# Kernel optimization log

Hardware: AMD Instinct MI355X
Metric: run time of the kernel (lower is better)

The kernel has to match this reference:

```python
import jax, jax.numpy as jnp
import numpy as np

K_HIDDEN = 512
N_POS = 24
N_COLOR = 6
EPS = 1e-5


def setup_inputs() -> dict:
    key = jax.random.key(0)
    k1, k2 = jax.random.split(key)
    B = 1024
    x = jax.random.normal(k1, (B, N_POS, N_COLOR * K_HIDDEN), dtype=jnp.float32)
    # kaiming-uniform-ish scale for the (k_out, k_in, 2) weight
    fan_in = K_HIDDEN * 2
    bound = float(np.sqrt(6.0 / fan_in))
    conv_weight = jax.random.uniform(k2, (K_HIDDEN, K_HIDDEN, 2), dtype=jnp.float32,
                                     minval=-bound, maxval=bound)
    conv_bias = jnp.zeros((K_HIDDEN,), dtype=jnp.float32)
    norm_weight = jnp.ones((K_HIDDEN,), dtype=jnp.float32)
    norm_bias = jnp.zeros((K_HIDDEN,), dtype=jnp.float32)
    return {"x": x, "conv_weight": conv_weight, "conv_bias": conv_bias,
            "norm_weight": norm_weight, "norm_bias": norm_bias}


def _color_layernorm(x, gamma, beta):
    # x: (B, 24, 6*k); normalize over the full channel axis, affine tied per block of 6
    mean = jnp.mean(x, axis=-1, keepdims=True)
    var = jnp.mean(jnp.square(x - mean), axis=-1, keepdims=True)  # unbiased=False
    xn = (x - mean) * jax.lax.rsqrt(var + EPS)
    xn = xn.reshape(*x.shape[:-1], K_HIDDEN, N_COLOR)
    xn = xn * gamma[:, None] + beta[:, None]
    return xn.reshape(x.shape)


def _color_conv(x, weight, bias):
    # x: (B, 24, 6*k) -> (B, 24, k, 6)
    B = x.shape[0]
    xr = x.reshape(B, N_POS, K_HIDDEN, N_COLOR)
    alpha = weight[:, :, 0] - weight[:, :, 1]   # (k_out, k_in)
    beta_w = weight[:, :, 1]                    # (k_out, k_in)
    term1 = jnp.einsum('bikd,ok->biod', xr, alpha)      # per-color linear
    x_sum = xr.sum(axis=3)                               # (B, 24, k_in)
    term2 = jnp.einsum('bik,ok->bio', x_sum, beta_w)     # color-sum linear
    out = term1 + term2[..., None] + bias[None, None, :, None]
    return out.reshape(B, N_POS, K_HIDDEN * N_COLOR)


def reference(x, conv_weight, conv_bias, norm_weight, norm_bias):
    h = _color_layernorm(x, norm_weight, norm_bias)
    h = _color_conv(h, conv_weight, conv_bias)
    return x + jax.nn.relu(h)
```

## Files before the change

### kernel.cpp

```cpp
#include <hip/hip_runtime.h>
#include <stdint.h>
#include <stddef.h>

#define KH   512
#define DF   3072
#define EPSF 1e-5f
#define PPB  8
#define ROWS 48
#define TSS  516

typedef __attribute__((ext_vector_type(4))) float f32x4;
typedef __attribute__((ext_vector_type(2))) float f32x2;
typedef __attribute__((ext_vector_type(8))) short bf16x8;
typedef __attribute__((ext_vector_type(4))) unsigned int u32x4;

__device__ __forceinline__ unsigned short f2bf(float f) {
  union { float f; unsigned u; } c; c.f = f;
  unsigned u = c.u;
  u += 0x7fffu + ((u >> 16) & 1u);
  return (unsigned short)(u >> 16);
}
__device__ __forceinline__ unsigned short f2bf_trunc(float f) {
  union { float f; unsigned u; } c; c.f = f;
  return (unsigned short)(c.u >> 16);
}
__device__ __forceinline__ float bf2f(unsigned short u) {
  union { unsigned u; float f; } c; c.u = ((unsigned)u) << 16;
  return c.f;
}
__device__ __forceinline__ float bfl(unsigned u) {
  union { unsigned u; float f; } c; c.u = u << 16;
  return c.f;
}
__device__ __forceinline__ float bfh(unsigned u) {
  union { unsigned u; float f; } c; c.u = u & 0xffff0000u;
  return c.f;
}

__global__ __launch_bounds__(256) void prep_w(const float* __restrict__ cw,
                                              const float* __restrict__ cb,
                                              const float* __restrict__ nw,
                                              const float* __restrict__ nb,
                                              unsigned char* __restrict__ wbt,
                                              float* __restrict__ c12) {
  const int o = blockIdx.x;
  const int t = threadIdx.x;
  const int wn = o >> 6, nn = (o >> 4) & 3, co = o & 15;
  float c1 = 0.f, c2 = 0.f;
  for (int k = t; k < KH; k += 256) {
    float w0 = cw[o * 1024 + 2 * k];
    float w1 = cw[o * 1024 + 2 * k + 1];
    float a  = w0 - w1;
    float g  = nw[k], b = nb[k];
    int s = k >> 5, kin = k & 31, h = kin >> 3, e = kin & 7;
    size_t base = (size_t)(((wn * 16 + s) * 4 + nn)) * 1024 + (h * 16 + co) * 16 + e * 2;
    *(unsigned short*)(wbt + base)          = f2bf(a * g);
    *(unsigned short*)(wbt + base + 524288) = f2bf(w1 * g);
    float tt = a + 6.f * w1;
    c1 += tt * b;
    c2 += tt * g;
  }
  #pragma unroll
  for (int off = 32; off >= 1; off >>= 1) {
    c1 += __shfl_xor(c1, off);
    c2 += __shfl_xor(c2, off);
  }
  __shared__ float s1[4], s2[4];
  int wid = t >> 6, lane = t & 63;
  if (lane == 0) { s1[wid] = c1; s2[wid] = c2; }
  __syncthreads();
  if (t == 0) {
    c12[o]      = s1[0] + s1[1] + s1[2] + s1[3] + cb[o];
    c12[KH + o] = s2[0] + s2[1] + s2[2] + s2[3];
  }
}

__global__ __launch_bounds__(512, 4) void fused_main(
    const float* __restrict__ x,
    const unsigned char* __restrict__ wbt,
    const float* __restrict__ c12,
    float* __restrict__ out)
{
  __shared__ unsigned char As[ROWS * 1024];
  __shared__ unsigned char Sx[PPB * 1024];
  __shared__ float Ts[PPB * TSS];
  __shared__ float st[PPB * 2];

  const int tid  = threadIdx.x;
  const int lane = tid & 63;
  const int wid  = tid >> 6;
  const int co   = lane & 15;
  const int h    = lane >> 4;
  const int rvb  = h << 2;
  const size_t r0 = (size_t)blockIdx.x * PPB;

  const unsigned char* wA = wbt + (size_t)wid * 65536;
  bf16x8 bvA[4], bvB[4];

  {
    const float* xb = x + r0 * DF;
    f32x4 q[12];
    #pragma unroll
    for (int i = 0; i < 12; i++) q[i] = *(const f32x4*)(xb + i * 2048 + tid * 4);

    #pragma unroll
    for (int n = 0; n < 4; n++)
      bvA[n] = *(const bf16x8*)(wA + n * 1024 + lane * 16);

    #pragma unroll
    for (int i = 0; i < 12; i++) {
      int base = i * 2048 + tid * 4;
      int pl   = base / 3072;
      int rem  = base - pl * 3072;
      int k0   = rem / 6;
      int d0   = rem - k0 * 6;
      #pragma unroll
      for (int e = 0; e < 4; e++) {
        int d = d0 + e, k = k0;
        if (d >= 6) { d -= 6; k += 1; }
        int row  = pl * 6 + d;
        int byte = row * 1024 + ((((k >> 3) ^ (row & 7)) << 4)) + (k & 7) * 2;
        *(unsigned short*)(As + byte) = f2bf_trunc(q[i][e]);
      }
    }
  }
  __syncthreads();

  {
    float vals[48];
    #pragma unroll
    for (int d = 0; d < 6; d++) {
      int row = wid * 6 + d;
      u32x4 v = *(const u32x4*)(As + row * 1024 + ((lane ^ (row & 7)) << 4));
      #pragma unroll
      for (int jj = 0; jj < 4; jj++) {
        vals[d * 8 + 2 * jj]     = bfl(v[jj]);
        vals[d * 8 + 2 * jj + 1] = bfh(v[jj]);
      }
    }
    float s = 0.f, sq = 0.f;
    #pragma unroll
    for (int i = 0; i < 48; i++) { s += vals[i]; sq += vals[i] * vals[i]; }
    #pragma unroll
    for (int off = 32; off >= 1; off >>= 1) {
      s  += __shfl_xor(s,  off);
      sq += __shfl_xor(sq, off);
    }
    float mean = s * (1.f / 3072.f);
    float var  = sq * (1.f / 3072.f) - mean * mean;
    float rstd = rsqrtf(var + EPSF);
    if (lane == 0) { st[2 * wid] = mean; st[2 * wid + 1] = rstd; }
    bf16x8 sv;
    #pragma unroll
    for (int g = 0; g < 8; g++) {
      float ss = vals[g] + vals[8 + g] + vals[16 + g] + vals[24 + g] +
                 vals[32 + g] + vals[40 + g];
      sv[g] = (short)f2bf(ss);
    }
    *(bf16x8*)(Sx + wid * 1024 + ((lane ^ (wid & 7)) << 4)) = sv;
  }
  __syncthreads();

  f32x4 acc1[3][4];
  #pragma unroll
  for (int m = 0; m < 3; m++)
    #pragma unroll
    for (int n = 0; n < 4; n++) acc1[m][n] = (f32x4){0.f, 0.f, 0.f, 0.f};

  int arow[3], ar7[3];
  #pragma unroll
  for (int m = 0; m < 3; m++) {
    int row = m * 16 + co;
    arow[m] = row * 1024;  ar7[m] = row & 7;
  }

  {
    bf16x8 afA[3], afB[3];
    #pragma unroll
    for (int m = 0; m < 3; m++)
      afA[m] = *(const bf16x8*)(As + arow[m] + ((h ^ ar7[m]) << 4));

    #pragma unroll 1
    for (int s = 0; s < 16; s += 2) {
      {
        int g6 = (s + 1) * 4 + h;
        #pragma unroll
        for (int m = 0; m < 3; m++)
          afB[m] = *(const bf16x8*)(As + arow[m] + ((g6 ^ ar7[m]) << 4));
        const unsigned char* pn = wA + (size_t)(s + 1) * 4096;
        #pragma unroll
        for (int n = 0; n < 4; n++)
          bvB[n] = *(const bf16x8*)(pn + n * 1024 + lane * 16);
      }
      #pragma unroll
      for (int m = 0; m < 3; m++)
        #pragma unroll
        for (int n = 0; n < 4; n++)
          acc1[m][n] = __builtin_amdgcn_mfma_f32_16x16x32_bf16(afA[m], bvA[n], acc1[m][n], 0, 0, 0);
      if (s + 2 < 16) {
        int g6 = (s + 2) * 4 + h;
        #pragma unroll
        for (int m = 0; m < 3; m++)
          afA[m] = *(const bf16x8*)(As + arow[m] + ((g6 ^ ar7[m]) << 4));
        const unsigned char* pn2 = wA + (size_t)(s + 2) * 4096;
        #pragma unroll
        for (int n = 0; n < 4; n++)
          bvA[n] = *(const bf16x8*)(pn2 + n * 1024 + lane * 16);
      }
      #pragma unroll
      for (int m = 0; m < 3; m++)
        #pragma unroll
        for (int n = 0; n < 4; n++)
          acc1[m][n] = __builtin_amdgcn_mfma_f32_16x16x32_bf16(afB[m], bvB[n], acc1[m][n], 0, 0, 0);
    }
  }

  {
    f32x4 acc2[4];
    #pragma unroll
    for (int n = 0; n < 4; n++) acc2[n] = (f32x4){0.f, 0.f, 0.f, 0.f};
    const unsigned char* wB2 = wbt + 524288 + (size_t)wid * 65536;
    const int sxr = (co & 7);
    bf16x8 cA[4], cB[4];
    bf16x8 a2A, a2B;
    #pragma unroll
    for (int n = 0; n < 4; n++)
      cA[n] = *(const bf16x8*)(wB2 + n * 1024 + lane * 16);
    a2A = *(const bf16x8*)(Sx + sxr * 1024 + ((h ^ sxr) << 4));

    #pragma unroll 1
    for (int s = 0; s < 16; s += 2) {
      {
        int g6 = (s + 1) * 4 + h;
        a2B = *(const bf16x8*)(Sx + sxr * 1024 + ((g6 ^ sxr) << 4));
        const unsigned char* pn = wB2 + (size_t)(s + 1) * 4096;
        #pragma unroll
        for (int n = 0; n < 4; n++)
          cB[n] = *(const bf16x8*)(pn + n * 1024 + lane * 16);
      }
      #pragma unroll
      for (int n = 0; n < 4; n++)
        acc2[n] = __builtin_amdgcn_mfma_f32_16x16x32_bf16(a2A, cA[n], acc2[n], 0, 0, 0);
      if (s + 2 < 16) {
        int g6 = (s + 2) * 4 + h;
        a2A = *(const bf16x8*)(Sx + sxr * 1024 + ((g6 ^ sxr) << 4));
        const unsigned char* pn2 = wB2 + (size_t)(s + 2) * 4096;
        #pragma unroll
        for (int n = 0; n < 4; n++)
          cA[n] = *(const bf16x8*)(pn2 + n * 1024 + lane * 16);
      }
      #pragma unroll
      for (int n = 0; n < 4; n++)
        acc2[n] = __builtin_amdgcn_mfma_f32_16x16x32_bf16(a2B, cB[n], acc2[n], 0, 0, 0);
    }
    if (h < 2) {
      #pragma unroll
      for (int n = 0; n < 4; n++)
        #pragma unroll
        for (int v = 0; v < 4; v++)
          Ts[(rvb + v) * TSS + wid * 64 + n * 16 + co] = acc2[n][v];
    }
  }

  #pragma unroll
  for (int n = 0; n < 4; n++) {
    const int o = wid * 64 + n * 16 + co;
    const float C1 = c12[o];
    const float C2 = c12[KH + o];
    const int swzo = o >> 3;
    const int ob2 = (o & 7) * 2;
    #pragma unroll
    for (int m = 0; m < 3; m++) {
      int j0  = m * 16 + rvb;
      int pl0 = j0 / 6;
      int d0  = j0 - pl0 * 6;
      float mean0 = st[2 * pl0], rstd0 = st[2 * pl0 + 1];
      float t20   = Ts[pl0 * TSS + o];
      float cc0   = C1 - mean0 * rstd0 * C2;
      if (d0 < 3) {
        f32x4 ov;
        #pragma unroll
        for (int v = 0; v < 4; v++) {
          int j = j0 + v;
          unsigned short rx = *(const unsigned short*)(
              As + j * 1024 + ((swzo ^ (j & 7)) << 4) + ob2);
          ov[v] = bf2f(rx) + fmaxf(rstd0 * (acc1[m][n][v] + t20) + cc0, 0.f);
        }
        *(f32x4*)(out + (r0 + pl0) * DF + o * 6 + d0) = ov;
      } else {
        int pl1 = pl0 + 1;
        float mean1 = st[2 * pl1], rstd1 = st[2 * pl1 + 1];
        float t21   = Ts[pl1 * TSS + o];
        float cc1   = C1 - mean1 * rstd1 * C2;
        f32x2 o0, o1;
        #pragma unroll
        for (int v = 0; v < 2; v++) {
          int j = j0 + v;
          unsigned short rx = *(const unsigned short*)(
              As + j * 1024 + ((swzo ^ (j & 7)) << 4) + ob2);
          o0[v] = bf2f(rx) + fmaxf(rstd0 * (acc1[m][n][v] + t20) + cc0, 0.f);
        }
        #pragma unroll
        for (int v = 2; v < 4; v++) {
          int j = j0 + v;
          unsigned short rx = *(const unsigned short*)(
              As + j * 1024 + ((swzo ^ (j & 7)) << 4) + ob2);
          o1[v - 2] = bf2f(rx) + fmaxf(rstd1 * (acc1[m][n][v] + t21) + cc1, 0.f);
        }
        *(f32x2*)(out + (r0 + pl0) * DF + o * 6 + 4) = o0;
        *(f32x2*)(out + (r0 + pl1) * DF + o * 6)     = o1;
      }
    }
  }
}

extern "C" void kernel_launch(void* const* d_in, const int* in_sizes, int n_in,
                              void* d_out, int out_size, void* d_ws, size_t ws_size,
                              hipStream_t stream) {
  (void)n_in; (void)out_size; (void)ws_size;
  const float* x  = (const float*)d_in[0];
  const float* cw = (const float*)d_in[1];
  const float* cb = (const float*)d_in[2];
  const float* nw = (const float*)d_in[3];
  const float* nb = (const float*)d_in[4];
  float* out = (float*)d_out;

  unsigned char* wbt = (unsigned char*)d_ws;
  float* c12 = (float*)((char*)d_ws + (size_t)1024 * 1024);

  prep_w<<<512, 256, 0, stream>>>(cw, cb, nw, nb, wbt, c12);

  const int R = in_sizes[0] / DF;
  fused_main<<<R / PPB, 512, 0, stream>>>(x, wbt, c12, out);
}
```

Before: 238.4 us.

## Load one row per wave directly and drop scattered LDS staging pass

Each wave now loads its own position row contiguously, 48 floats per lane, and computes LayerNorm statistics and color sums straight from registers. It then writes the bf16 A tile with vectorized 16-byte LDS stores instead of per-element 2-byte scattered stores, and one __syncthreads plus the LDS re-read are removed. It also wraps the MFMA bursts in s_setprio to favour matrix issue over competing waves. The global load pattern per instruction changes from fully coalesced across the block to per-lane 192-byte strided chunks. The color sum now uses truncating rather than rounding bf16 conversion, which slightly changes numerics.

```diff
diff --git a/kernel.cpp b/kernel.cpp
--- a/kernel.cpp
+++ b/kernel.cpp
@@ -12,7 +12,6 @@
 typedef __attribute__((ext_vector_type(4))) float f32x4;
 typedef __attribute__((ext_vector_type(2))) float f32x2;
 typedef __attribute__((ext_vector_type(8))) short bf16x8;
-typedef __attribute__((ext_vector_type(4))) unsigned int u32x4;
 
 __device__ __forceinline__ unsigned short f2bf(float f) {
   union { float f; unsigned u; } c; c.f = f;
@@ -26,14 +25,6 @@
 }
 __device__ __forceinline__ float bf2f(unsigned short u) {
   union { unsigned u; float f; } c; c.u = ((unsigned)u) << 16;
-  return c.f;
-}
-__device__ __forceinline__ float bfl(unsigned u) {
-  union { unsigned u; float f; } c; c.u = u << 16;
-  return c.f;
-}
-__device__ __forceinline__ float bfh(unsigned u) {
-  union { unsigned u; float f; } c; c.u = u & 0xffff0000u;
   return c.f;
 }
 
@@ -98,49 +89,24 @@
   bf16x8 bvA[4], bvB[4];
 
   {
-    const float* xb = x + r0 * DF;
+    const float* xr = x + (size_t)(r0 + wid) * DF + lane * 48;
     f32x4 q[12];
     #pragma unroll
-    for (int i = 0; i < 12; i++) q[i] = *(const f32x4*)(xb + i * 2048 + tid * 4);
+    for (int i = 0; i < 12; i++) q[i] = *(const f32x4*)(xr + i * 4);
 
     #pragma unroll
     for (int n = 0; n < 4; n++)
       bvA[n] = *(const bf16x8*)(wA + n * 1024 + lane * 16);
 
+    float vv[48];
     #pragma unroll
     for (int i = 0; i < 12; i++) {
-      int base = i * 2048 + tid * 4;
-      int pl   = base / 3072;
-      int rem  = base - pl * 3072;
-      int k0   = rem / 6;
-      int d0   = rem - k0 * 6;
-      #pragma unroll
-      for (int e = 0; e < 4; e++) {
-        int d = d0 + e, k = k0;
-        if (d >= 6) { d -= 6; k += 1; }
-        int row  = pl * 6 + d;
-        int byte = row * 1024 + ((((k >> 3) ^ (row & 7)) << 4)) + (k & 7) * 2;
-        *(unsigned short*)(As + byte) = f2bf_trunc(q[i][e]);
-      }
-    }
-  }
-  __syncthreads();
-
-  {
-    float vals[48];
-    #pragma unroll
-    for (int d = 0; d < 6; d++) {
-      int row = wid * 6 + d;
-      u32x4 v = *(const u32x4*)(As + row * 1024 + ((lane ^ (row & 7)) << 4));
-      #pragma unroll
-      for (int jj = 0; jj < 4; jj++) {
-        vals[d * 8 + 2 * jj]     = bfl(v[jj]);
-        vals[d * 8 + 2 * jj + 1] = bfh(v[jj]);
-      }
+      vv[4 * i] = q[i].x; vv[4 * i + 1] = q[i].y;
+      vv[4 * i + 2] = q[i].z; vv[4 * i + 3] = q[i].w;
     }
     float s = 0.f, sq = 0.f;
     #pragma unroll
-    for (int i = 0; i < 48; i++) { s += vals[i]; sq += vals[i] * vals[i]; }
+    for (int i = 0; i < 48; i++) { s += vv[i]; sq += vv[i] * vv[i]; }
     #pragma unroll
     for (int off = 32; off >= 1; off >>= 1) {
       s  += __shfl_xor(s,  off);
@@ -150,12 +116,21 @@
     float var  = sq * (1.f / 3072.f) - mean * mean;
     float rstd = rsqrtf(var + EPSF);
     if (lane == 0) { st[2 * wid] = mean; st[2 * wid + 1] = rstd; }
+
+    #pragma unroll
+    for (int d = 0; d < 6; d++) {
+      int row = wid * 6 + d;
+      bf16x8 v;
+      #pragma unroll
+      for (int g = 0; g < 8; g++) v[g] = (short)f2bf_trunc(vv[g * 6 + d]);
+      *(bf16x8*)(As + row * 1024 + ((lane ^ (row & 7)) << 4)) = v;
+    }
     bf16x8 sv;
     #pragma unroll
     for (int g = 0; g < 8; g++) {
-      float ss = vals[g] + vals[8 + g] + vals[16 + g] + vals[24 + g] +
-                 vals[32 + g] + vals[40 + g];
-      sv[g] = (short)f2bf(ss);
+      float ss = vv[g * 6] + vv[g * 6 + 1] + vv[g * 6 + 2] +
+                 vv[g * 6 + 3] + vv[g * 6 + 4] + vv[g * 6 + 5];
+      sv[g] = (short)f2bf_trunc(ss);
     }
     *(bf16x8*)(Sx + wid * 1024 + ((lane ^ (wid & 7)) << 4)) = sv;
   }
@@ -192,11 +167,13 @@
         for (int n = 0; n < 4; n++)
           bvB[n] = *(const bf16x8*)(pn + n * 1024 + lane * 16);
       }
+      __builtin_amdgcn_s_setprio(1);
       #pragma unroll
       for (int m = 0; m < 3; m++)
         #pragma unroll
         for (int n = 0; n < 4; n++)
           acc1[m][n] = __builtin_amdgcn_mfma_f32_16x16x32_bf16(afA[m], bvA[n], acc1[m][n], 0, 0, 0);
+      __builtin_amdgcn_s_setprio(0);
       if (s + 2 < 16) {
         int g6 = (s + 2) * 4 + h;
         #pragma unroll
@@ -207,11 +184,13 @@
         for (int n = 0; n < 4; n++)
           bvA[n] = *(const bf16x8*)(pn2 + n * 1024 + lane * 16);
       }
+      __builtin_amdgcn_s_setprio(1);
       #pragma unroll
       for (int m = 0; m < 3; m++)
         #pragma unroll
         for (int n = 0; n < 4; n++)
           acc1[m][n] = __builtin_amdgcn_mfma_f32_16x16x32_bf16(afB[m], bvB[n], acc1[m][n], 0, 0, 0);
+      __builtin_amdgcn_s_setprio(0);
     }
   }
 
@@ -238,9 +217,11 @@
         for (int n = 0; n < 4; n++)
           cB[n] = *(const bf16x8*)(pn + n * 1024 + lane * 16);
       }
+      __builtin_amdgcn_s_setprio(1);
       #pragma unroll
       for (int n = 0; n < 4; n++)
         acc2[n] = __builtin_amdgcn_mfma_f32_16x16x32_bf16(a2A, cA[n], acc2[n], 0, 0, 0);
+      __builtin_amdgcn_s_setprio(0);
       if (s + 2 < 16) {
         int g6 = (s + 2) * 4 + h;
         a2A = *(const bf16x8*)(Sx + sxr * 1024 + ((g6 ^ sxr) << 4));
@@ -249,9 +230,11 @@
         for (int n = 0; n < 4; n++)
           cA[n] = *(const bf16x8*)(pn2 + n * 1024 + lane * 16);
       }
+      __builtin_amdgcn_s_setprio(1);
       #pragma unroll
       for (int n = 0; n < 4; n++)
         acc2[n] = __builtin_amdgcn_mfma_f32_16x16x32_bf16(a2B, cB[n], acc2[n], 0, 0, 0);
+      __builtin_amdgcn_s_setprio(0);
     }
     if (h < 2) {
       #pragma unroll
```

Result: no change. 234.1 us (-1.8%).
